# Kernel tuning notes

Measured on AMD Instinct MI355X. Metric: run time of the kernel, lower is better.

## Reference

```python
import jax, jax.numpy as jnp
import numpy as np

NUM_HEADS = 4
WINDOW = 3

def setup_inputs() -> dict:
    key = jax.random.key(0)
    ks = jax.random.split(key, 6)
    B, V, C, H, W = 4, 6, 256, 32, 32
    s = 0.02
    return {
        "x": jax.random.normal(ks[0], (B, V, C, H, W), jnp.float32),
        "Wq": jax.random.normal(ks[1], (C, C), jnp.float32) * s,
        "bq": jnp.zeros((C,), jnp.float32),
        "Wk": jax.random.normal(ks[2], (V * C, C), jnp.float32) * s,
        "bk": jnp.zeros((C,), jnp.float32),
        "Wv": jax.random.normal(ks[3], (V * C, C), jnp.float32) * s,
        "bv": jnp.zeros((C,), jnp.float32),
        "Wo": jax.random.normal(ks[4], (C, C), jnp.float32) * s,
        "bo": jnp.zeros((C,), jnp.float32),
    }

def reference(x, Wq, bq, Wk, bk, Wv, bv, Wo, bo):
    B, V, C, H, W = x.shape
    HW = H * W
    S = HW * V  # query sequence length
    nh = NUM_HEADS
    hd = C // nh
    # q: [B, V, H, W, C] -> [B, S, C]
    q_in = jnp.transpose(x, (0, 1, 3, 4, 2)).reshape(B, S, C)
    # k/v input: [B, H, W, V, C] -> [B, HW, V*C]
    kv_in = jnp.transpose(x, (0, 3, 4, 1, 2)).reshape(B, HW, V * C)
    q = q_in @ Wq + bq
    k = kv_in @ Wk + bk
    v = kv_in @ Wv + bv
    q = q.reshape(B, S, nh, hd).transpose(0, 2, 1, 3)    # [B, nh, S, hd]
    k = k.reshape(B, HW, nh, hd).transpose(0, 2, 1, 3)   # [B, nh, HW, hd]
    v = v.reshape(B, HW, nh, hd).transpose(0, 2, 1, 3)   # [B, nh, HW, hd]
    logits = jnp.einsum("bhqd,bhkd->bhqk", q, k) / jnp.sqrt(jnp.float32(hd))
    # Faithful mask: row i has ones in columns [max(0,i-W), i+W] (clipped to HW cols);
    # it is ADDED as mask * -1e9, masking OUT the diagonal window (as in source).
    i = jnp.arange(S)[:, None]
    j = jnp.arange(HW)[None, :]
    mask = ((j >= i - WINDOW) & (j < i + WINDOW + 1)).astype(logits.dtype)
    logits = logits + mask * (-1e9)
    attn = jax.nn.softmax(logits, axis=-1)
    out = jnp.einsum("bhqk,bhkd->bhqd", attn, v)         # [B, nh, S, hd]
    out = out.transpose(0, 2, 1, 3).reshape(B, S, C)
    out = out @ Wo + bo
    return x.reshape(B * V, C, H, W) + out.reshape(B * V, C, H, W)
```

## Files before the change

kernel.cpp:

```cpp
#include <hip/hip_runtime.h>
#include <cstddef>

namespace {

constexpr int B=4, V=6, C=256, HWS=1024, S=6144, NH=4, HD=64, VC=1536;

typedef short short8  __attribute__((ext_vector_type(8)));
typedef short short4v __attribute__((ext_vector_type(4)));
typedef float f32x4   __attribute__((ext_vector_type(4)));

__device__ inline short f2bf(float f){
  union{float f; unsigned u;} v; v.f=f;
  unsigned r = v.u + 0x7fffu + ((v.u>>16)&1u);
  return (short)(r>>16);
}
__device__ inline unsigned fbits(float f){
  union{float f; unsigned u;} v; v.f=f; return v.u;
}

typedef const __attribute__((address_space(1))) unsigned* gas_t;
typedef __attribute__((address_space(3))) unsigned* las_t;
__device__ inline void gll(const void* g, void* l){
  __builtin_amdgcn_global_load_lds((gas_t)g, (las_t)l, 16, 0, 0);
}

__device__ inline void tr_tile(const float* in, int inRow, short* out, int outRow,
                               int r0, int c0, int t){
  const int tx=t&15, ty=t>>4;
  float a[4][4];
  #pragma unroll
  for(int i=0;i<4;i++){
    const float4 f=*(const float4*)(in + (size_t)(r0+ty*4+i)*inRow + c0 + tx*4);
    a[i][0]=f.x; a[i][1]=f.y; a[i][2]=f.z; a[i][3]=f.w;
  }
  #pragma unroll
  for(int j=0;j<4;j++){
    short4v o4;
    #pragma unroll
    for(int i=0;i<4;i++) o4[i]=f2bf(a[i][j]);
    *(short4v*)(out + (size_t)(c0+tx*4+j)*outRow + r0+ty*4) = o4;
  }
}

__global__ __launch_bounds__(256) void prep(const float* __restrict__ x,
                                            const float* __restrict__ Wq, const float* __restrict__ Wk,
                                            const float* __restrict__ Wv, const float* __restrict__ Wo,
                                            short* __restrict__ xb, short* __restrict__ WqT,
                                            short* __restrict__ WkT, short* __restrict__ WvT,
                                            short* __restrict__ WoT){
  const int blk=blockIdx.x;
  if(blk<1536){
    const int bx=blk&15, by=(blk>>4)&3, bv=blk>>6;
    tr_tile(x + (size_t)bv*C*HWS, HWS, xb + (size_t)bv*HWS*C, C, by*64, bx*64, threadIdx.x);
  } else {
    const int idx=blk-1536;
    const int tile=idx%96, z=idx/96;
    const float* in; short* out; int R;
    if(z==0){in=Wq; out=WqT; R=C;}
    else if(z==1){in=Wo; out=WoT; R=C;}
    else if(z==2){in=Wk; out=WkT; R=VC;}
    else         {in=Wv; out=WvT; R=VC;}
    const int tilesC=C/64, ntiles=(R/64)*tilesC;
    if(tile>=ntiles) return;
    tr_tile(in, C, out, R, (tile/tilesC)*64, (tile%tilesC)*64, threadIdx.x);
  }
}

template<int MODE>
__device__ inline void qo_body(const short* __restrict__ A, const short* __restrict__ BT,
                               const float* __restrict__ bias, const float* __restrict__ xres,
                               void* __restrict__ outv, short* As, short* Bs, int n0, int r0){
  const int t=threadIdx.x, lane=t&63, w=t>>6, quad=lane>>4, ln=lane&15;
  f32x4 acc[2][4];
  #pragma unroll
  for(int rt=0;rt<2;rt++)
    #pragma unroll
    for(int nt=0;nt<4;nt++) acc[rt][nt]=(f32x4)0.f;

  for(int k0=0;k0<C;k0+=64){
    if(k0) __syncthreads();
    { const int r=t>>1, c=(t&1)*32;
      const short* p = A + (size_t)(r0+r)*C + k0 + c;
      #pragma unroll
      for(int j=0;j<4;j++) *(short8*)&As[r*72+c+j*8] = *(const short8*)(p+j*8);
    }
    { const int n=t>>2, c=(t&3)*16;
      const short* p = BT + (size_t)(n0+n)*C + k0 + c;
      *(short8*)&Bs[n*72+c]   = *(const short8*)p;
      *(short8*)&Bs[n*72+c+8] = *(const short8*)(p+8);
    }
    __syncthreads();
    #pragma unroll
    for(int s=0;s<2;s++){
      short8 af0=*(short8*)&As[(w*32+ln)*72    + s*32+quad*8];
      short8 af1=*(short8*)&As[(w*32+16+ln)*72 + s*32+quad*8];
      #pragma unroll
      for(int nt=0;nt<4;nt++){
        const short8 bf=*(short8*)&Bs[(nt*16+ln)*72 + s*32+quad*8];
        acc[0][nt]=__builtin_amdgcn_mfma_f32_16x16x32_bf16(af0,bf,acc[0][nt],0,0,0);
        acc[1][nt]=__builtin_amdgcn_mfma_f32_16x16x32_bf16(af1,bf,acc[1][nt],0,0,0);
      }
    }
  }

  constexpr float QSCALE = 0.18033688011112042f;
  float bcol[4];
  #pragma unroll
  for(int nt=0;nt<4;nt++) bcol[nt]=bias[n0+nt*16+ln];
  #pragma unroll
  for(int rt=0;rt<2;rt++)
    #pragma unroll
    for(int nt=0;nt<4;nt++)
      #pragma unroll
      for(int i=0;i<4;i++){
        const int row=r0+w*32+rt*16+quad*4+i, col=n0+nt*16+ln;
        const float vv=acc[rt][nt][i]+bcol[nt];
        if constexpr(MODE==0) ((short*)outv)[(size_t)row*C+col]=f2bf(vv*QSCALE);
        else ((float*)outv)[(size_t)row*C+col]=vv + xres[(size_t)row*C+col];
      }
}

__global__ __launch_bounds__(256) void proj(const short* __restrict__ xb,
                                            const short* __restrict__ WqT, const short* __restrict__ WkT,
                                            const short* __restrict__ WvT,
                                            const float* __restrict__ bq, const float* __restrict__ bk,
                                            const float* __restrict__ bv,
                                            short* __restrict__ qb, short* __restrict__ Kpack,
                                            short* __restrict__ Vpack){
  __shared__ __align__(16) short sh[13824];
  const int blk=blockIdx.x;
  const int t=threadIdx.x, lane=t&63, w=t>>6, quad=lane>>4, ln=lane&15;

  if(blk>=256){
    const int qblk=blk-256;
    qo_body<0>(xb, WqT, bq, nullptr, qb, sh, sh+9216, (qblk&3)*64, (qblk>>2)*128);
    return;
  }

  short* As=sh; short* Bk=sh+4608; short* Bv=sh+9216;
  const int n0=(blk&3)*64, r0=(blk>>2)*64;
  const int b=r0>>10, hw0=r0&1023;
  const int h=n0>>6, bh=b*NH+h;

  f32x4 ak[4], av[4];
  #pragma unroll
  for(int nt=0;nt<4;nt++){ ak[nt]=(f32x4)0.f; av[nt]=(f32x4)0.f; }

  const int sr=t>>2, sc=(t&3)*16;
  for(int k0=0;k0<VC;k0+=64){
    if(k0) __syncthreads();
    const int v=k0>>8, c0=k0&255;
    { const short* p = xb + (size_t)((b*V+v)*HWS + hw0+sr)*C + c0 + sc;
      *(short8*)&As[sr*72+sc]   = *(const short8*)p;
      *(short8*)&As[sr*72+sc+8] = *(const short8*)(p+8); }
    { const short* p = WkT + (size_t)(n0+sr)*VC + k0 + sc;
      *(short8*)&Bk[sr*72+sc]   = *(const short8*)p;
      *(short8*)&Bk[sr*72+sc+8] = *(const short8*)(p+8); }
    { const short* p = WvT + (size_t)(n0+sr)*VC + k0 + sc;
      *(short8*)&Bv[sr*72+sc]   = *(const short8*)p;
      *(short8*)&Bv[sr*72+sc+8] = *(const short8*)(p+8); }
    __syncthreads();
    #pragma unroll
    for(int s=0;s<2;s++){
      const short8 af=*(short8*)&As[(w*16+ln)*72 + s*32+quad*8];
      #pragma unroll
      for(int nt=0;nt<4;nt++){
        const short8 kf=*(short8*)&Bk[(nt*16+ln)*72 + s*32+quad*8];
        const short8 vf=*(short8*)&Bv[(nt*16+ln)*72 + s*32+quad*8];
        ak[nt]=__builtin_amdgcn_mfma_f32_16x16x32_bf16(af,kf,ak[nt],0,0,0);
        av[nt]=__builtin_amdgcn_mfma_f32_16x16x32_bf16(af,vf,av[nt],0,0,0);
      }
    }
  }

  float bkc[4], bvc[4];
  #pragma unroll
  for(int nt=0;nt<4;nt++){ bkc[nt]=bk[n0+nt*16+ln]; bvc[nt]=bv[n0+nt*16+ln]; }

  {
    short* vq = Vpack + ((size_t)(bh*64 + (hw0>>4) + w))*1024;
    #pragma unroll
    for(int nt=0;nt<4;nt++){
      short4v vp;
      #pragma unroll
      for(int i=0;i<4;i++) vp[i]=f2bf(av[nt][i]+bvc[nt]);
      *(short4v*)(vq + nt*256 + lane*4) = vp;
    }
  }

  __syncthreads();
  #pragma unroll
  for(int nt=0;nt<4;nt++)
    #pragma unroll
    for(int i=0;i<4;i++)
      As[(w*16+quad*4+i)*72 + nt*16+ln] = f2bf(ak[nt][i]+bkc[nt]);
  __syncthreads();
  {
    short* kp = Kpack + ((size_t)(bh*64 + (hw0>>4) + w))*1024;
    #pragma unroll
    for(int half=0; half<2; half++){
      const short8 f = *(short8*)&As[(w*16+ln)*72 + half*32 + quad*8];
      *(short8*)(kp + half*512 + lane*8) = f;
    }
  }
}

__global__ __launch_bounds__(512,4) void attn_k(const short* __restrict__ q, const short* __restrict__ Kpack,
                                                const short* __restrict__ Vpack, short* __restrict__ ao){
  __shared__ __align__(16) char smem[34816];
  short* KV   = (short*)smem;
  float* obuf = (float*)smem;
  float* lbuf = (float*)(smem + 33792);

  const int blk=blockIdx.x;
  const int bh=(blk&7)*2 + ((blk>>3)&1);
  const int qt=blk>>4;
  const int b=bh>>2, h=bh&3;
  const int s0=qt*128;
  const int t=threadIdx.x, lane=t&63, w=t>>6, quad=lane>>4, ln=lane&15;
  const int wq=w&3, wk=w>>2;

  short8 qf[2][2];
  #pragma unroll
  for(int ntl=0;ntl<2;ntl++)
    #pragma unroll
    for(int s=0;s<2;s++)
      qf[ntl][s]=*(const short8*)&q[(size_t)(b*S+s0+wq*32+ntl*16+ln)*C + h*HD + s*32+quad*8];

  f32x4 o[4][2];
  #pragma unroll
  for(int dt=0;dt<4;dt++)
    #pragma unroll
    for(int ntl=0;ntl<2;ntl++) o[dt][ntl]=(f32x4)0.f;
  f32x4 l4[2];
  l4[0]=(f32x4)0.f; l4[1]=(f32x4)0.f;

  const short* Kt = Kpack + (size_t)bh*65536;
  const short* Vt = Vpack + (size_t)bh*65536;
  const f32x4 z4=(f32x4)0.f;
  const int rb = s0 + wq*32;

  gll(Kt + w*512 + lane*8, KV + w*512);
  gll(Vt + 0*4096 + w*512 + lane*8, KV + 4096 + w*512);
  __syncthreads();

  #pragma unroll 1
  for(int TI=0; TI<16; TI++){
    if(TI<15){
      const int nb=(TI+1)&1;
      gll(Kt + (size_t)(TI+1)*4096 + w*512 + lane*8, KV + nb*8192 + w*512);
      gll(Vt + (size_t)(TI+1)*4096 + w*512 + lane*8, KV + nb*8192 + 4096 + w*512);
    }
    const short* Kb = KV + (TI&1)*8192;
    const short* Vb = Kb + 4096;

    const short8 kf00=*(const short8*)&Kb[wk*2048 + lane*8];
    const short8 kf01=*(const short8*)&Kb[wk*2048 + 512 + lane*8];
    const short8 kf10=*(const short8*)&Kb[wk*2048 + 1024 + lane*8];
    const short8 kf11=*(const short8*)&Kb[wk*2048 + 1536 + lane*8];

    f32x4 sa[2][2];
    #pragma unroll
    for(int ntl=0;ntl<2;ntl++){
      sa[0][ntl]=__builtin_amdgcn_mfma_f32_16x16x32_bf16(kf00,qf[ntl][0],z4,0,0,0);
      sa[0][ntl]=__builtin_amdgcn_mfma_f32_16x16x32_bf16(kf01,qf[ntl][1],sa[0][ntl],0,0,0);
      sa[1][ntl]=__builtin_amdgcn_mfma_f32_16x16x32_bf16(kf10,qf[ntl][0],z4,0,0,0);
      sa[1][ntl]=__builtin_amdgcn_mfma_f32_16x16x32_bf16(kf11,qf[ntl][1],sa[1][ntl],0,0,0);
    }

    short4v vf[2][4];
    #pragma unroll
    for(int kt=0;kt<2;kt++)
      #pragma unroll
      for(int dt=0;dt<4;dt++)
        vf[kt][dt]=*(const short4v*)&Vb[wk*2048 + kt*1024 + dt*256 + lane*4];

    const int kmin=TI*64 + wk*32;
    if(kmin+31 >= rb-3 && kmin <= rb+34){
      #pragma unroll
      for(int kt=0;kt<2;kt++)
        #pragma unroll
        for(int ntl=0;ntl<2;ntl++){
          const int ig=rb+ntl*16+ln;
          #pragma unroll
          for(int i=0;i<4;i++){
            const int jg=kmin+kt*16+quad*4+i;
            if((unsigned)(jg-ig+3)<=6u) sa[kt][ntl][i]=-100.f;
          }
        }
    }

    short4v pt[2][2];
    #pragma unroll
    for(int kt=0;kt<2;kt++)
      #pragma unroll
      for(int ntl=0;ntl<2;ntl++){
        f32x4 pv;
        #pragma unroll
        for(int i=0;i<4;i++) pv[i]=__builtin_amdgcn_exp2f(sa[kt][ntl][i]);
        l4[ntl]+=pv;
        union{ short4v s; unsigned u[2]; } P;
        P.u[0]=__builtin_amdgcn_perm(fbits(pv[1]), fbits(pv[0]), 0x07060302u);
        P.u[1]=__builtin_amdgcn_perm(fbits(pv[3]), fbits(pv[2]), 0x07060302u);
        pt[kt][ntl]=P.s;
      }

    #pragma unroll
    for(int kt=0;kt<2;kt++)
      #pragma unroll
      for(int dt=0;dt<4;dt++)
        #pragma unroll
        for(int ntl=0;ntl<2;ntl++)
          o[dt][ntl]=__builtin_amdgcn_mfma_f32_16x16x16bf16_1k(vf[kt][dt],pt[kt][ntl],o[dt][ntl],0,0,0);

    __syncthreads();
  }

  float l[2];
  #pragma unroll
  for(int ntl=0;ntl<2;ntl++){
    l[ntl]=l4[ntl][0]+l4[ntl][1]+l4[ntl][2]+l4[ntl][3];
    l[ntl]+=__shfl_xor(l[ntl],16);
    l[ntl]+=__shfl_xor(l[ntl],32);
  }
  if(quad==0){
    lbuf[w*32+ln]    = l[0];
    lbuf[w*32+16+ln] = l[1];
  }
  if(wk==0){
    #pragma unroll
    for(int dt=0;dt<4;dt++)
      #pragma unroll
      for(int ntl=0;ntl<2;ntl++)
        #pragma unroll
        for(int i=0;i<4;i++)
          obuf[(dt*16+quad*4+i)*132 + wq*32+ntl*16+ln] = o[dt][ntl][i];
  }
  __syncthreads();
  if(wk==1){
    #pragma unroll
    for(int dt=0;dt<4;dt++)
      #pragma unroll
      for(int ntl=0;ntl<2;ntl++)
        #pragma unroll
        for(int i=0;i<4;i++)
          obuf[(dt*16+quad*4+i)*132 + wq*32+ntl*16+ln] += o[dt][ntl][i];
  }
  __syncthreads();

  {
    const int row=t>>2, dg=t&3;
    const float linv=1.0f/(lbuf[(row>>5)*32 + (row&31)] + lbuf[(4+(row>>5))*32 + (row&31)]);
    short tmp[16];
    #pragma unroll
    for(int j=0;j<16;j++) tmp[j]=f2bf(obuf[(dg*16+j)*132+row]*linv);
    short* op = ao + (size_t)(b*S+s0+row)*C + h*HD + dg*16;
    *(short8*)op     = *(short8*)&tmp[0];
    *(short8*)(op+8) = *(short8*)&tmp[8];
  }
}

__global__ __launch_bounds__(256) void o_gemm(const short* __restrict__ A, const short* __restrict__ BT,
                                              const float* __restrict__ bias, const float* __restrict__ xres,
                                              float* __restrict__ out){
  __shared__ __align__(16) short sh[13824];
  qo_body<1>(A, BT, bias, xres, out, sh, sh+9216, (int)(blockIdx.x&3)*64, (int)(blockIdx.x>>2)*128);
}

}

extern "C" void kernel_launch(void* const* d_in, const int* in_sizes, int n_in,
                              void* d_out, int out_size, void* d_ws, size_t ws_size,
                              hipStream_t stream) {
  const float* x  = (const float*)d_in[0];
  const float* Wq = (const float*)d_in[1];
  const float* bq = (const float*)d_in[2];
  const float* Wk = (const float*)d_in[3];
  const float* bk = (const float*)d_in[4];
  const float* Wv = (const float*)d_in[5];
  const float* bv = (const float*)d_in[6];
  const float* Wo = (const float*)d_in[7];
  const float* bo = (const float*)d_in[8];
  float* out = (float*)d_out;

  char* p = (char*)d_ws;
  const size_t szBS=(size_t)B*S*C*2, szK=(size_t)B*HWS*C*2;
  short* xb   =(short*)p; p+=szBS;
  short* qb   =(short*)p; p+=szBS;
  short* aob  =(short*)p; p+=szBS;
  short* Kpack=(short*)p; p+=szK;
  short* Vpack=(short*)p; p+=szK;
  short* WqT=(short*)p; p+=(size_t)C*C*2;
  short* WoT=(short*)p; p+=(size_t)C*C*2;
  short* WkT=(short*)p; p+=(size_t)C*VC*2;
  short* WvT=(short*)p; p+=(size_t)C*VC*2;

  prep<<<dim3(1920), 256, 0, stream>>>(x, Wq,Wk,Wv,Wo, xb, WqT,WkT,WvT,WoT);
  proj<<<dim3(1024), 256, 0, stream>>>(xb, WqT,WkT,WvT, bq,bk,bv, qb, Kpack, Vpack);
  attn_k<<<dim3(B*NH*(S/128)), 512, 0, stream>>>(qb, Kpack, Vpack, aob);
  o_gemm<<<dim3(4*((B*S)/128)), 256, 0, stream>>>(aob, WoT, bo, x, out);
}
```

Baseline: 184.3 us.

## Double-buffer projection GEMM tiles via direct global-to-LDS async loads

The Q/O GEMM body and the fused K/V projection now stage their A and B tiles with global_load_lds (direct global-to-LDS) into two LDS buffers. The next k-slice is prefetched while MFMAs run on the current one, which removes the register round-trip and the serialized load-then-compute pattern. The LDS row stride drops from 72 to 64 so the tiles match the async-load layout. That may add bank conflicts on the fragment reads, and shared memory per block grows to 48 KB, which could reduce occupancy.

```diff
diff --git a/kernel.cpp b/kernel.cpp
--- a/kernel.cpp
+++ b/kernel.cpp
@@ -69,7 +69,7 @@
 template<int MODE>
 __device__ inline void qo_body(const short* __restrict__ A, const short* __restrict__ BT,
                                const float* __restrict__ bias, const float* __restrict__ xres,
-                               void* __restrict__ outv, short* As, short* Bs, int n0, int r0){
+                               void* __restrict__ outv, short* sh, int n0, int r0){
   const int t=threadIdx.x, lane=t&63, w=t>>6, quad=lane>>4, ln=lane&15;
   f32x4 acc[2][4];
   #pragma unroll
@@ -77,30 +77,37 @@
     #pragma unroll
     for(int nt=0;nt<4;nt++) acc[rt][nt]=(f32x4)0.f;
 
-  for(int k0=0;k0<C;k0+=64){
-    if(k0) __syncthreads();
-    { const int r=t>>1, c=(t&1)*32;
-      const short* p = A + (size_t)(r0+r)*C + k0 + c;
-      #pragma unroll
-      for(int j=0;j<4;j++) *(short8*)&As[r*72+c+j*8] = *(const short8*)(p+j*8);
-    }
-    { const int n=t>>2, c=(t&3)*16;
-      const short* p = BT + (size_t)(n0+n)*C + k0 + c;
-      *(short8*)&Bs[n*72+c]   = *(const short8*)p;
-      *(short8*)&Bs[n*72+c+8] = *(const short8*)(p+8);
-    }
-    __syncthreads();
+  const int sr=w*8+(lane>>3), scc=(lane&7)*8;
+  auto stage=[&](int it,int bufi){
+    const int k0=it*64;
+    short* dst = sh + bufi*12288;
+    const short* Asrc = A + (size_t)r0*C + k0;
+    #pragma unroll
+    for(int cc=0; cc<4; cc++)
+      gll(Asrc + (size_t)(sr+cc*32)*C + scc, dst + cc*2048 + w*512);
+    const short* Bsrc = BT + (size_t)n0*C + k0;
+    gll(Bsrc + (size_t)sr*C + scc,      dst + 8192 + w*512);
+    gll(Bsrc + (size_t)(sr+32)*C + scc, dst + 8192 + 2048 + w*512);
+  };
+
+  stage(0,0);
+  __syncthreads();
+  for(int it=0; it<4; it++){
+    if(it<3) stage(it+1,(it+1)&1);
+    const short* As_=sh+(it&1)*12288;
+    const short* Bs_=As_+8192;
     #pragma unroll
     for(int s=0;s<2;s++){
-      short8 af0=*(short8*)&As[(w*32+ln)*72    + s*32+quad*8];
-      short8 af1=*(short8*)&As[(w*32+16+ln)*72 + s*32+quad*8];
+      const short8 af0=*(const short8*)&As_[(w*32+ln)*64    + s*32+quad*8];
+      const short8 af1=*(const short8*)&As_[(w*32+16+ln)*64 + s*32+quad*8];
       #pragma unroll
       for(int nt=0;nt<4;nt++){
-        const short8 bf=*(short8*)&Bs[(nt*16+ln)*72 + s*32+quad*8];
+        const short8 bf=*(const short8*)&Bs_[(nt*16+ln)*64 + s*32+quad*8];
         acc[0][nt]=__builtin_amdgcn_mfma_f32_16x16x32_bf16(af0,bf,acc[0][nt],0,0,0);
         acc[1][nt]=__builtin_amdgcn_mfma_f32_16x16x32_bf16(af1,bf,acc[1][nt],0,0,0);
       }
     }
+    __syncthreads();
   }
 
   constexpr float QSCALE = 0.18033688011112042f;
@@ -127,17 +134,16 @@
                                             const float* __restrict__ bv,
                                             short* __restrict__ qb, short* __restrict__ Kpack,
                                             short* __restrict__ Vpack){
-  __shared__ __align__(16) short sh[13824];
+  __shared__ __align__(16) short sh[24576];
   const int blk=blockIdx.x;
   const int t=threadIdx.x, lane=t&63, w=t>>6, quad=lane>>4, ln=lane&15;
 
   if(blk>=256){
     const int qblk=blk-256;
-    qo_body<0>(xb, WqT, bq, nullptr, qb, sh, sh+9216, (qblk&3)*64, (qblk>>2)*128);
+    qo_body<0>(xb, WqT, bq, nullptr, qb, sh, (qblk&3)*64, (qblk>>2)*128);
     return;
   }
 
-  short* As=sh; short* Bk=sh+4608; short* Bv=sh+9216;
   const int n0=(blk&3)*64, r0=(blk>>2)*64;
   const int b=r0>>10, hw0=r0&1023;
   const int h=n0>>6, bh=b*NH+h;
@@ -146,31 +152,40 @@
   #pragma unroll
   for(int nt=0;nt<4;nt++){ ak[nt]=(f32x4)0.f; av[nt]=(f32x4)0.f; }
 
-  const int sr=t>>2, sc=(t&3)*16;
-  for(int k0=0;k0<VC;k0+=64){
-    if(k0) __syncthreads();
-    const int v=k0>>8, c0=k0&255;
-    { const short* p = xb + (size_t)((b*V+v)*HWS + hw0+sr)*C + c0 + sc;
-      *(short8*)&As[sr*72+sc]   = *(const short8*)p;
-      *(short8*)&As[sr*72+sc+8] = *(const short8*)(p+8); }
-    { const short* p = WkT + (size_t)(n0+sr)*VC + k0 + sc;
-      *(short8*)&Bk[sr*72+sc]   = *(const short8*)p;
-      *(short8*)&Bk[sr*72+sc+8] = *(const short8*)(p+8); }
-    { const short* p = WvT + (size_t)(n0+sr)*VC + k0 + sc;
-      *(short8*)&Bv[sr*72+sc]   = *(const short8*)p;
-      *(short8*)&Bv[sr*72+sc+8] = *(const short8*)(p+8); }
-    __syncthreads();
+  const int sr=w*8+(lane>>3), scc=(lane&7)*8;
+  auto stageKV=[&](int it,int bufi){
+    const int k0=it*64, v=k0>>8, c0=k0&255;
+    short* dst = sh + bufi*12288;
+    const short* As_src = xb + (size_t)((b*V+v)*HWS + hw0)*C + c0;
+    gll(As_src + (size_t)sr*C + scc,       dst + w*512);
+    gll(As_src + (size_t)(sr+32)*C + scc,  dst + 2048 + w*512);
+    const short* Bk_src = WkT + (size_t)n0*VC + k0;
+    gll(Bk_src + (size_t)sr*VC + scc,      dst + 4096 + w*512);
+    gll(Bk_src + (size_t)(sr+32)*VC + scc, dst + 4096 + 2048 + w*512);
+    const short* Bv_src = WvT + (size_t)n0*VC + k0;
+    gll(Bv_src + (size_t)sr*VC + scc,      dst + 8192 + w*512);
+    gll(Bv_src + (size_t)(sr+32)*VC + scc, dst + 8192 + 2048 + w*512);
+  };
+
+  stageKV(0,0);
+  __syncthreads();
+  for(int it=0; it<24; it++){
+    if(it<23) stageKV(it+1,(it+1)&1);
+    const short* As_=sh+(it&1)*12288;
+    const short* Bk_=As_+4096;
+    const short* Bv_=As_+8192;
     #pragma unroll
     for(int s=0;s<2;s++){
-      const short8 af=*(short8*)&As[(w*16+ln)*72 + s*32+quad*8];
+      const short8 af=*(const short8*)&As_[(w*16+ln)*64 + s*32+quad*8];
       #pragma unroll
       for(int nt=0;nt<4;nt++){
-        const short8 kf=*(short8*)&Bk[(nt*16+ln)*72 + s*32+quad*8];
-        const short8 vf=*(short8*)&Bv[(nt*16+ln)*72 + s*32+quad*8];
+        const short8 kf=*(const short8*)&Bk_[(nt*16+ln)*64 + s*32+quad*8];
+        const short8 vf=*(const short8*)&Bv_[(nt*16+ln)*64 + s*32+quad*8];
         ak[nt]=__builtin_amdgcn_mfma_f32_16x16x32_bf16(af,kf,ak[nt],0,0,0);
         av[nt]=__builtin_amdgcn_mfma_f32_16x16x32_bf16(af,vf,av[nt],0,0,0);
       }
     }
+    __syncthreads();
   }
 
   float bkc[4], bvc[4];
@@ -193,13 +208,13 @@
   for(int nt=0;nt<4;nt++)
     #pragma unroll
     for(int i=0;i<4;i++)
-      As[(w*16+quad*4+i)*72 + nt*16+ln] = f2bf(ak[nt][i]+bkc[nt]);
+      sh[(w*16+quad*4+i)*72 + nt*16+ln] = f2bf(ak[nt][i]+bkc[nt]);
   __syncthreads();
   {
     short* kp = Kpack + ((size_t)(bh*64 + (hw0>>4) + w))*1024;
     #pragma unroll
     for(int half=0; half<2; half++){
-      const short8 f = *(short8*)&As[(w*16+ln)*72 + half*32 + quad*8];
+      const short8 f = *(short8*)&sh[(w*16+ln)*72 + half*32 + quad*8];
       *(short8*)(kp + half*512 + lane*8) = f;
     }
   }
@@ -241,7 +256,7 @@
   const int rb = s0 + wq*32;
 
   gll(Kt + w*512 + lane*8, KV + w*512);
-  gll(Vt + 0*4096 + w*512 + lane*8, KV + 4096 + w*512);
+  gll(Vt + w*512 + lane*8, KV + 4096 + w*512);
   __syncthreads();
 
   #pragma unroll 1
@@ -363,8 +378,8 @@
 __global__ __launch_bounds__(256) void o_gemm(const short* __restrict__ A, const short* __restrict__ BT,
                                               const float* __restrict__ bias, const float* __restrict__ xres,
                                               float* __restrict__ out){
-  __shared__ __align__(16) short sh[13824];
-  qo_body<1>(A, BT, bias, xres, out, sh, sh+9216, (int)(blockIdx.x&3)*64, (int)(blockIdx.x>>2)*128);
+  __shared__ __align__(16) short sh[24576];
+  qo_body<1>(A, BT, bias, xres, out, sh, (int)(blockIdx.x&3)*64, (int)(blockIdx.x>>2)*128);
 }
 
 }
```

Result: faster. 169.8 us (-7.9%).
